# Kernel optimization log

Hardware: AMD Instinct MI355X
Metric: run time of the kernel (lower is better)

Reference implementation:

```python
import jax, jax.numpy as jnp
import numpy as np

B1, B2, D = 8192, 12288, 128


def setup_inputs() -> dict:
    key = jax.random.key(0)
    k1, k2 = jax.random.split(key)
    desc1 = jax.random.normal(k1, (B1, D), dtype=jnp.float32)
    desc2 = jax.random.normal(k2, (B2, D), dtype=jnp.float32)
    return {"desc1": desc1, "desc2": desc2}


def reference(desc1, desc2):
    # Pairwise L2 distance (torch.cdist, p=2) via the expanded form to avoid
    sq1 = jnp.sum(desc1 * desc1, axis=1, keepdims=True)          # (B1, 1)
    sq2 = jnp.sum(desc2 * desc2, axis=1)                          # (B2,)
    cost = jnp.sqrt(jnp.maximum(sq1 + sq2 - 2.0 * (desc1 @ desc2.T), 0.0))  # (B1, B2)

    b1, b2 = cost.shape
    ms = min(b1, b2)

    match_dists = jnp.min(cost, axis=1)    # (B1,) row minima
    idxs_in_2 = jnp.argmin(cost, axis=1)   # (B1,)
    match_dists2 = jnp.min(cost, axis=0)   # (B2,) col minima
    idxs_in_1 = jnp.argmin(cost, axis=0)   # (B2,)

    minsize_idxs = jnp.arange(ms)
    if b1 <= b2:  # static shape comparison -> Python if is fine
        mutual_nns = minsize_idxs == idxs_in_1[idxs_in_2][:ms]
        dists = match_dists[:ms]
        matches_idxs = jnp.stack([minsize_idxs, idxs_in_2[:ms]], axis=1)
    else:
        mutual_nns = minsize_idxs == idxs_in_2[idxs_in_1][:ms]
        dists = match_dists2[:ms]
        matches_idxs = jnp.stack([idxs_in_1[:ms], minsize_idxs], axis=1)

    # jit-compatible fixed-size output: non-mutual rows are masked with
    # dist=+inf and idx=-1 instead of boolean-compressed as in torch.
    match_dists_out = jnp.where(mutual_nns, dists, jnp.inf).reshape(-1, 1)  # (ms, 1)
    matches_idxs_out = jnp.where(mutual_nns[:, None], matches_idxs, -1)      # (ms, 2)
    return match_dists_out, matches_idxs_out, mutual_nns
```

## Files before the change

### kernel.cpp

```cpp
#include <hip/hip_runtime.h>
#include <math.h>

#define NB1 8192
#define NB2 12288
#define DD  128

typedef unsigned long long u64;
typedef unsigned short ushort_t;
typedef __attribute__((ext_vector_type(8))) short short8;
typedef __attribute__((ext_vector_type(8))) _Float16 half8;
typedef __attribute__((ext_vector_type(4))) float f32x4;

__device__ __forceinline__ float bigf() { return __uint_as_float(0x7F7F0000u); }
__device__ __forceinline__ u64 umin64(u64 a, u64 b) { return a < b ? a : b; }
__device__ __forceinline__ unsigned umin32(unsigned a, unsigned b) { return a < b ? a : b; }

__device__ __forceinline__ ushort_t bf_rn(float x) {
    unsigned u = __float_as_uint(x);
    return (ushort_t)((u + 0x7FFFu + ((u >> 16) & 1u)) >> 16);
}
__device__ __forceinline__ float bf_up(ushort_t h) {
    return __uint_as_float(((unsigned)h) << 16);
}
__device__ __forceinline__ int fswz(int r) { return (r + (r >> 2)) & 3; }
__device__ __forceinline__ half8 ld8h(const _Float16* p) { return *(const half8*)p; }

__global__ __launch_bounds__(256) void prep_kernel(
    const float* __restrict__ d1, const float* __restrict__ d2,
    float* __restrict__ sq1, float* __restrict__ sq2,
    u64* __restrict__ rowmin, u64* __restrict__ colmin) {
    int t = blockIdx.x * 256 + threadIdx.x;
    if (t < NB1) {
        rowmin[t] = ~0ull;
        const float4* p = (const float4*)(d1 + (size_t)t * DD);
        float s = 0.f;
        #pragma unroll
        for (int c = 0; c < DD / 4; ++c) {
            float4 v = p[c];
            s = fmaf(v.x, v.x, s); s = fmaf(v.y, v.y, s);
            s = fmaf(v.z, v.z, s); s = fmaf(v.w, v.w, s);
        }
        sq1[t] = s;
    }
    if (t < NB2) {
        colmin[t] = ~0ull;
        const float4* p = (const float4*)(d2 + (size_t)t * DD);
        float s = 0.f;
        #pragma unroll
        for (int c = 0; c < DD / 4; ++c) {
            float4 v = p[c];
            s = fmaf(v.x, v.x, s); s = fmaf(v.y, v.y, s);
            s = fmaf(v.z, v.z, s); s = fmaf(v.w, v.w, s);
        }
        sq2[t] = s;
    }
}

__global__ __launch_bounds__(256) void split_ext16_kernel(
    const float* __restrict__ d1, const float* __restrict__ d2,
    _Float16* __restrict__ Af, _Float16* __restrict__ Bf) {
    int t = blockIdx.x * 256 + threadIdx.x;
    int lane = t & 63;
    int task = t >> 6;
    bool isA = task < 6144;
    int lt = isA ? task : task - 6144;
    int rb = lt / 12;
    int kc = lt - rb * 12;
    int region = kc >> 2;
    int row = rb * 16 + (lane & 15);
    int kst = (kc & 3) * 32 + (lane >> 4) * 8;
    const float* src = (isA ? d1 : d2) + (size_t)row * DD + kst;
    _Float16* dst = (isA ? Af : Bf) + ((size_t)lt * 512 + lane * 8);

    bool wantM = isA ? (region == 1) : (region == 2);
    half8 V;
    #pragma unroll
    for (int e = 0; e < 8; ++e) {
        float x = src[e];
        _Float16 hf = (_Float16)x;
        float h = (float)hf;
        float v;
        if (region == 0)      v = x;
        else if (wantM)       v = (x - h) * 256.0f;
        else                  v = h * 0.00390625f;
        V[e] = (_Float16)v;
    }
    *(half8*)dst = V;
}

__global__ __launch_bounds__(256) void mfma_tile8_kernel(
    const _Float16* __restrict__ Af, const _Float16* __restrict__ Bf,
    const float* __restrict__ sq1, const float* __restrict__ sq2,
    u64* __restrict__ rowmin, u64* __restrict__ colmin)
{
    const int bid  = blockIdx.x;
    const int xcd  = bid & 7;
    const int t_   = bid >> 3;
    const int kch  = t_ >> 6;
    const int wdn  = t_ & 63;
    const int j0b  = (kch * 8 + (wdn & 7)) * 128;
    const int i0b  = (xcd * 8 + (wdn >> 3)) * 128;

    const int tid  = threadIdx.x;
    const int lane = tid & 63;
    const int wid  = tid >> 6;
    const int wr   = wid >> 1;
    const int wc   = wid & 1;
    const int lrow = lane & 15;
    const int lg   = lane >> 4;

    const _Float16* abase = Af + ((size_t)((i0b >> 4) + wr * 4) * 6144) + lane * 8;
    const _Float16* bbase = Bf + ((size_t)((j0b >> 4) + wc * 4) * 6144) + lane * 8;

    f32x4 acc[4][4];
    #pragma unroll
    for (int mi = 0; mi < 4; ++mi)
        #pragma unroll
        for (int ni = 0; ni < 4; ++ni)
            acc[mi][ni] = (f32x4){0.f, 0.f, 0.f, 0.f};

    #pragma unroll 1
    for (int kc = 0; kc < 12; ++kc) {
        const int ko = kc * 512;
        half8 bfr[4];
        #pragma unroll
        for (int ni = 0; ni < 4; ++ni)
            bfr[ni] = ld8h(bbase + ni * 6144 + ko);
        half8 a0, a1;
        a0 = ld8h(abase + ko);
        #pragma unroll
        for (int mi = 0; mi < 4; ++mi) {
            if (mi < 3)
                a1 = ld8h(abase + (mi + 1) * 6144 + ko);
            #pragma unroll
            for (int ni = 0; ni < 4; ++ni)
                acc[mi][ni] = __builtin_amdgcn_mfma_f32_16x16x32_f16(a0, bfr[ni], acc[mi][ni], 0, 0, 0);
            a0 = a1;
        }
    }

    float q2v[4];
    #pragma unroll
    for (int ni = 0; ni < 4; ++ni)
        q2v[ni] = sq2[j0b + wc * 64 + ni * 16 + lrow];
    float4 q1v[4];
    #pragma unroll
    for (int mi = 0; mi < 4; ++mi)
        q1v[mi] = *(const float4*)(sq1 + i0b + wr * 64 + mi * 16 + 4 * lg);

    float    cmin[4];
    unsigned cidx[4];
    #pragma unroll
    for (int ni = 0; ni < 4; ++ni) { cmin[ni] = __uint_as_float(0x7F800000u); cidx[ni] = 0xFFFFFFFFu; }

    #pragma unroll
    for (int mi = 0; mi < 4; ++mi) {
        const float* q1p = (const float*)&q1v[mi];
        #pragma unroll
        for (int r = 0; r < 4; ++r) {
            const float    q1 = q1p[r];
            const unsigned irow = (unsigned)(i0b + wr * 64 + mi * 16 + 4 * lg + r);
            float    rbest = 0.f;
            unsigned rbn = 0;
            #pragma unroll
            for (int ni = 0; ni < 4; ++ni) {
                float d = acc[mi][ni][r];
                float t = fmaf(-2.f, d, q2v[ni]);
                float c = fmaf(-2.f, d, q1);
                if (ni == 0) { rbest = t; }
                else if (t < rbest) { rbest = t; rbn = (unsigned)ni; }
                if (c < cmin[ni]) { cmin[ni] = c; cidx[ni] = irow; }
            }
            float g = rbest;
            #pragma unroll
            for (int mask = 8; mask; mask >>= 1)
                g = fminf(g, __shfl_xor(g, mask));
            unsigned jc = (rbest == g)
                ? (unsigned)(j0b + wc * 64 + rbn * 16 + lrow) : 0xFFFFFFFFu;
            #pragma unroll
            for (int mask = 8; mask; mask >>= 1)
                jc = umin32(jc, (unsigned)__shfl_xor((int)jc, mask));
            if (lrow == 0) {
                float d2 = g + q1;
                u64 pk = ((u64)__float_as_uint(d2) << 32) | jc;
                atomicMin(&rowmin[irow], pk);
            }
        }
    }

    #pragma unroll
    for (int ni = 0; ni < 4; ++ni) {
        float d2 = cmin[ni] + q2v[ni];
        u64 pk = ((u64)__float_as_uint(d2) << 32) | cidx[ni];
        pk = umin64(pk, __shfl_xor(pk, 16));
        pk = umin64(pk, __shfl_xor(pk, 32));
        if (lane < 16)
            atomicMin(&colmin[j0b + wc * 64 + ni * 16 + lrow], pk);
    }
}

__global__ __launch_bounds__(256) void mfma_tile_kernel(
    const float* __restrict__ d1, const float* __restrict__ d2,
    const float* __restrict__ sq1, const float* __restrict__ sq2,
    u64* __restrict__ rowmin, u64* __restrict__ colmin)
{
    __shared__ __align__(16) short lds[6 * 4096];
    const int tid = threadIdx.x;
    const int i0b = blockIdx.y * 128;
    const int j0b = blockIdx.x * 128;
    const int srow  = tid >> 1;
    const int shalf = tid & 1;
    const int sfr   = fswz(srow);
    const int sg0   = ((2 * shalf) ^ sfr) * 8;
    const int sg1   = ((2 * shalf + 1) ^ sfr) * 8;
    const float* gA = d1 + (size_t)(i0b + srow) * DD + shalf * 16;
    const float* gB = d2 + (size_t)(j0b + srow) * DD + shalf * 16;
    short* wA = lds + srow * 32;
    short* wB = lds + 3 * 4096 + srow * 32;
    const int lane = tid & 63;
    const int wid  = tid >> 6;
    const int wr   = wid >> 1;
    const int wc   = wid & 1;
    const int lrow = lane & 15;
    const int lg   = lane >> 4;
    const int gx   = (lg ^ fswz(lrow)) * 8;
    const int aoff = (wr * 64 + lrow) * 32 + gx;
    const int boff = 3 * 4096 + (wc * 64 + lrow) * 32 + gx;

    f32x4 acc[4][4];
    #pragma unroll
    for (int mi = 0; mi < 4; ++mi)
        #pragma unroll
        for (int ni = 0; ni < 4; ++ni)
            acc[mi][ni] = (f32x4){0.f, 0.f, 0.f, 0.f};

    for (int kc = 0; kc < 4; ++kc) {
        {
            const float* sp = gA + kc * 32;
            short8 H0, M0, L0, H1, M1, L1;
            #pragma unroll
            for (int e = 0; e < 8; ++e) {
                float x = sp[e];
                ushort_t h = bf_rn(x); float r1 = x - bf_up(h);
                ushort_t m = bf_rn(r1); float r2 = r1 - bf_up(m);
                H0[e] = (short)h; M0[e] = (short)m; L0[e] = (short)bf_rn(r2);
            }
            #pragma unroll
            for (int e = 0; e < 8; ++e) {
                float x = sp[8 + e];
                ushort_t h = bf_rn(x); float r1 = x - bf_up(h);
                ushort_t m = bf_rn(r1); float r2 = r1 - bf_up(m);
                H1[e] = (short)h; M1[e] = (short)m; L1[e] = (short)bf_rn(r2);
            }
            *(short8*)(wA + sg0)        = H0;
            *(short8*)(wA + sg1)        = H1;
            *(short8*)(wA + 4096 + sg0) = M0;
            *(short8*)(wA + 4096 + sg1) = M1;
            *(short8*)(wA + 8192 + sg0) = L0;
            *(short8*)(wA + 8192 + sg1) = L1;
        }
        {
            const float* sp = gB + kc * 32;
            short8 H0, M0, L0, H1, M1, L1;
            #pragma unroll
            for (int e = 0; e < 8; ++e) {
                float x = sp[e];
                ushort_t h = bf_rn(x); float r1 = x - bf_up(h);
                ushort_t m = bf_rn(r1); float r2 = r1 - bf_up(m);
                H0[e] = (short)h; M0[e] = (short)m; L0[e] = (short)bf_rn(r2);
            }
            #pragma unroll
            for (int e = 0; e < 8; ++e) {
                float x = sp[8 + e];
                ushort_t h = bf_rn(x); float r1 = x - bf_up(h);
                ushort_t m = bf_rn(r1); float r2 = r1 - bf_up(m);
                H1[e] = (short)h; M1[e] = (short)m; L1[e] = (short)bf_rn(r2);
            }
            *(short8*)(wB + sg0)        = H0;
            *(short8*)(wB + sg1)        = H1;
            *(short8*)(wB + 4096 + sg0) = M0;
            *(short8*)(wB + 4096 + sg1) = M1;
            *(short8*)(wB + 8192 + sg0) = L0;
            *(short8*)(wB + 8192 + sg1) = L1;
        }
        __syncthreads();
        short8 af[3][4], bfr[3][4];
        #pragma unroll
        for (int c = 0; c < 3; ++c)
            #pragma unroll
            for (int t = 0; t < 4; ++t) {
                af[c][t]  = *(const short8*)(lds + c * 4096 + aoff + t * 512);
                bfr[c][t] = *(const short8*)(lds + c * 4096 + boff + t * 512);
            }
        #pragma unroll
        for (int mi = 0; mi < 4; ++mi)
            #pragma unroll
            for (int ni = 0; ni < 4; ++ni) {
                f32x4 a = acc[mi][ni];
                a = __builtin_amdgcn_mfma_f32_16x16x32_bf16(af[0][mi], bfr[0][ni], a, 0, 0, 0);
                a = __builtin_amdgcn_mfma_f32_16x16x32_bf16(af[0][mi], bfr[1][ni], a, 0, 0, 0);
                a = __builtin_amdgcn_mfma_f32_16x16x32_bf16(af[1][mi], bfr[0][ni], a, 0, 0, 0);
                a = __builtin_amdgcn_mfma_f32_16x16x32_bf16(af[0][mi], bfr[2][ni], a, 0, 0, 0);
                a = __builtin_amdgcn_mfma_f32_16x16x32_bf16(af[1][mi], bfr[1][ni], a, 0, 0, 0);
                a = __builtin_amdgcn_mfma_f32_16x16x32_bf16(af[2][mi], bfr[0][ni], a, 0, 0, 0);
                acc[mi][ni] = a;
            }
        __syncthreads();
    }

    float q2v[4];
    #pragma unroll
    for (int ni = 0; ni < 4; ++ni)
        q2v[ni] = sq2[j0b + wc * 64 + ni * 16 + lrow];
    float4 q1v[4];
    #pragma unroll
    for (int mi = 0; mi < 4; ++mi)
        q1v[mi] = *(const float4*)(sq1 + i0b + wr * 64 + mi * 16 + 4 * lg);

    float    cmin[4];
    unsigned cidx[4];
    #pragma unroll
    for (int ni = 0; ni < 4; ++ni) { cmin[ni] = __uint_as_float(0x7F800000u); cidx[ni] = 0xFFFFFFFFu; }

    #pragma unroll
    for (int mi = 0; mi < 4; ++mi) {
        const float* q1p = (const float*)&q1v[mi];
        #pragma unroll
        for (int r = 0; r < 4; ++r) {
            const float    q1 = q1p[r];
            const unsigned irow = (unsigned)(i0b + wr * 64 + mi * 16 + 4 * lg + r);
            float    rbest = 0.f;
            unsigned rbn = 0;
            #pragma unroll
            for (int ni = 0; ni < 4; ++ni) {
                float d = acc[mi][ni][r];
                float t = fmaf(-2.f, d, q2v[ni]);
                float c = fmaf(-2.f, d, q1);
                if (ni == 0) { rbest = t; }
                else if (t < rbest) { rbest = t; rbn = (unsigned)ni; }
                if (c < cmin[ni]) { cmin[ni] = c; cidx[ni] = irow; }
            }
            float g = rbest;
            #pragma unroll
            for (int mask = 8; mask; mask >>= 1)
                g = fminf(g, __shfl_xor(g, mask));
            unsigned jc = (rbest == g)
                ? (unsigned)(j0b + wc * 64 + rbn * 16 + lrow) : 0xFFFFFFFFu;
            #pragma unroll
            for (int mask = 8; mask; mask >>= 1)
                jc = umin32(jc, (unsigned)__shfl_xor((int)jc, mask));
            if (lrow == 0) {
                float d2 = g + q1;
                u64 pk = ((u64)__float_as_uint(d2) << 32) | jc;
                atomicMin(&rowmin[irow], pk);
            }
        }
    }
    #pragma unroll
    for (int ni = 0; ni < 4; ++ni) {
        float d2 = cmin[ni] + q2v[ni];
        u64 pk = ((u64)__float_as_uint(d2) << 32) | cidx[ni];
        pk = umin64(pk, __shfl_xor(pk, 16));
        pk = umin64(pk, __shfl_xor(pk, 32));
        if (lane < 16)
            atomicMin(&colmin[j0b + wc * 64 + ni * 16 + lrow], pk);
    }
}

__global__ __launch_bounds__(256) void final_kernel(
    const u64* __restrict__ rowmin, const u64* __restrict__ colmin,
    float* __restrict__ out) {
    int i = blockIdx.x * 256 + threadIdx.x;
    if (i >= NB1) return;
    u64 rm = rowmin[i];
    unsigned ju = (unsigned)(rm & 0xFFFFFFFFu);
    float d2 = __uint_as_float((unsigned)(rm >> 32));
    float dist = sqrtf(fmaxf(d2, 0.f));
    dist = fminf(dist, bigf());
    bool valid = (ju < (unsigned)NB2);
    int j = valid ? (int)ju : 0;
    u64 cm = colmin[j];
    int i2 = (int)(cm & 0xFFFFFFFFu);
    bool mut = valid && (i2 == i);
    out[i] = mut ? dist : bigf();
    out[NB1 + 2 * i]     = mut ? (float)i : -1.f;
    out[NB1 + 2 * i + 1] = mut ? (float)j : -1.f;
    out[NB1 + 2 * NB1 + i] = mut ? 1.f : 0.f;
}

extern "C" void kernel_launch(void* const* d_in, const int* in_sizes, int n_in,
                              void* d_out, int out_size, void* d_ws, size_t ws_size,
                              hipStream_t stream) {
    const float* d1 = (const float*)d_in[0];
    const float* d2 = (const float*)d_in[1];
    float* out = (float*)d_out;

    char* ws = (char*)d_ws;
    float* sq1    = (float*)(ws);
    float* sq2    = (float*)(ws + 32768);
    u64*   rowmin = (u64*)(ws + 81920);
    u64*   colmin = (u64*)(ws + 147456);
    _Float16* Af = (_Float16*)(ws + 245760);
    _Float16* Bf = (_Float16*)(ws + 245760 + 6291456);
    const size_t need = 245760 + 6291456 + 9437184;

    hipLaunchKernelGGL(prep_kernel, dim3((NB2 + 255) / 256), dim3(256), 0, stream,
                       d1, d2, sq1, sq2, rowmin, colmin);
    if (ws_size >= need) {
        hipLaunchKernelGGL(split_ext16_kernel, dim3(3840), dim3(256), 0, stream,
                           d1, d2, Af, Bf);
        hipLaunchKernelGGL(mfma_tile8_kernel, dim3(6144), dim3(256), 0, stream,
                           Af, Bf, sq1, sq2, rowmin, colmin);
    } else {
        hipLaunchKernelGGL(mfma_tile_kernel, dim3(NB2 / 128, NB1 / 128), dim3(256), 0, stream,
                           d1, d2, sq1, sq2, rowmin, colmin);
    }
    hipLaunchKernelGGL(final_kernel, dim3((NB1 + 255) / 256), dim3(256), 0, stream,
                       rowmin, colmin, out);
}
```

Measured before the change: 230.2 us.

## Stage fp16 split operands through LDS via direct global-to-LDS loads

The split kernel now writes each descriptor as one row-major 384-wide fp16 row, with the high part and the two scaled residual parts laid side by side. Before, the data was pre-packed into MFMA-fragment blocks. The GEMM kernel now uses global_load_lds to stage a 128x32 A tile and a 128x32 B tile per K step into swizzled shared memory, and all four waves read their fragments from there. The goal is to cut redundant global/L2 fragment loads, since previously each fragment was fetched separately by two waves. The cost is two block barriers per K step with a single LDS buffer and no overlap of load and compute.

```diff
diff --git a/kernel.cpp b/kernel.cpp
--- a/kernel.cpp
+++ b/kernel.cpp
@@ -4,6 +4,7 @@
 #define NB1 8192
 #define NB2 12288
 #define DD  128
+#define KE  384
 
 typedef unsigned long long u64;
 typedef unsigned short ushort_t;
@@ -24,6 +25,12 @@
 }
 __device__ __forceinline__ int fswz(int r) { return (r + (r >> 2)) & 3; }
 __device__ __forceinline__ half8 ld8h(const _Float16* p) { return *(const half8*)p; }
+
+__device__ __forceinline__ void gload_lds16(const void* g, void* l) {
+    __builtin_amdgcn_global_load_lds(
+        (const __attribute__((address_space(1))) unsigned*)g,
+        (__attribute__((address_space(3))) unsigned*)l, 16, 0, 0);
+}
 
 __global__ __launch_bounds__(256) void prep_kernel(
     const float* __restrict__ d1, const float* __restrict__ d2,
@@ -56,43 +63,43 @@
     }
 }
 
-__global__ __launch_bounds__(256) void split_ext16_kernel(
+__global__ __launch_bounds__(256) void split_kcat16_kernel(
     const float* __restrict__ d1, const float* __restrict__ d2,
-    _Float16* __restrict__ Af, _Float16* __restrict__ Bf) {
+    _Float16* __restrict__ Ap, _Float16* __restrict__ Bp) {
     int t = blockIdx.x * 256 + threadIdx.x;
-    int lane = t & 63;
-    int task = t >> 6;
-    bool isA = task < 6144;
-    int lt = isA ? task : task - 6144;
-    int rb = lt / 12;
-    int kc = lt - rb * 12;
-    int region = kc >> 2;
-    int row = rb * 16 + (lane & 15);
-    int kst = (kc & 3) * 32 + (lane >> 4) * 8;
-    const float* src = (isA ? d1 : d2) + (size_t)row * DD + kst;
-    _Float16* dst = (isA ? Af : Bf) + ((size_t)lt * 512 + lane * 8);
-
-    bool wantM = isA ? (region == 1) : (region == 2);
-    half8 V;
-    #pragma unroll
-    for (int e = 0; e < 8; ++e) {
-        float x = src[e];
-        _Float16 hf = (_Float16)x;
-        float h = (float)hf;
-        float v;
-        if (region == 0)      v = x;
-        else if (wantM)       v = (x - h) * 256.0f;
-        else                  v = h * 0.00390625f;
-        V[e] = (_Float16)v;
-    }
-    *(half8*)dst = V;
-}
-
-__global__ __launch_bounds__(256) void mfma_tile8_kernel(
-    const _Float16* __restrict__ Af, const _Float16* __restrict__ Bf,
+    int row = t >> 2, q = t & 3;
+    bool isA = row < NB1;
+    int r = isA ? row : row - NB1;
+    const float* src = (isA ? d1 : d2) + (size_t)r * DD + q * 32;
+    _Float16* dst = (isA ? Ap : Bp) + (size_t)r * KE + q * 32;
+
+    #pragma unroll
+    for (int v = 0; v < 4; ++v) {
+        half8 H, S1, S2;
+        #pragma unroll
+        for (int e = 0; e < 8; ++e) {
+            float x = src[v * 8 + e];
+            _Float16 hf = (_Float16)x;
+            float h = (float)hf;
+            _Float16 Mt = (_Float16)((x - h) * 256.0f);
+            _Float16 Ht = (_Float16)(h * 0.00390625f);
+            H[e] = hf;
+            S1[e] = isA ? Mt : Ht;
+            S2[e] = isA ? Ht : Mt;
+        }
+        *(half8*)(dst + v * 8)       = H;
+        *(half8*)(dst + 128 + v * 8) = S1;
+        *(half8*)(dst + 256 + v * 8) = S2;
+    }
+}
+
+__global__ __launch_bounds__(256) void mfma_lds9_kernel(
+    const _Float16* __restrict__ Ap, const _Float16* __restrict__ Bp,
     const float* __restrict__ sq1, const float* __restrict__ sq2,
     u64* __restrict__ rowmin, u64* __restrict__ colmin)
 {
+    __shared__ __align__(16) _Float16 lds[8192];
+
     const int bid  = blockIdx.x;
     const int xcd  = bid & 7;
     const int t_   = bid >> 3;
@@ -109,8 +116,23 @@
     const int lrow = lane & 15;
     const int lg   = lane >> 4;
 
-    const _Float16* abase = Af + ((size_t)((i0b >> 4) + wr * 4) * 6144) + lane * 8;
-    const _Float16* bbase = Bf + ((size_t)((j0b >> 4) + wc * 4) * 6144) + lane * 8;
+    const int srow0 = wid * 16 + (lane >> 2);
+    const int srow1 = 64 + srow0;
+    const int g0 = (lane & 3) ^ ((srow0 >> 1) & 3);
+    const int g1 = (lane & 3) ^ ((srow1 >> 1) & 3);
+    const _Float16* a0src = Ap + (size_t)(i0b + srow0) * KE + g0 * 8;
+    const _Float16* a1src = Ap + (size_t)(i0b + srow1) * KE + g1 * 8;
+    const _Float16* b0src = Bp + (size_t)(j0b + srow0) * KE + g0 * 8;
+    const _Float16* b1src = Bp + (size_t)(j0b + srow1) * KE + g1 * 8;
+    char* ldsA0 = (char*)lds + wid * 1024;
+    char* ldsA1 = (char*)lds + 4096 + wid * 1024;
+    char* ldsB0 = (char*)lds + 8192 + wid * 1024;
+    char* ldsB1 = (char*)lds + 12288 + wid * 1024;
+
+    const int arow = wr * 64 + lrow;
+    const int brow = wc * 64 + lrow;
+    const int aoff = arow * 32 + ((lg ^ ((arow >> 1) & 3)) * 8);
+    const int boff = 4096 + brow * 32 + ((lg ^ ((brow >> 1) & 3)) * 8);
 
     f32x4 acc[4][4];
     #pragma unroll
@@ -120,23 +142,27 @@
             acc[mi][ni] = (f32x4){0.f, 0.f, 0.f, 0.f};
 
     #pragma unroll 1
-    for (int kc = 0; kc < 12; ++kc) {
-        const int ko = kc * 512;
-        half8 bfr[4];
+    for (int T = 0; T < 12; ++T) {
+        const int ko = T * 32;
+        gload_lds16(a0src + ko, ldsA0);
+        gload_lds16(a1src + ko, ldsA1);
+        gload_lds16(b0src + ko, ldsB0);
+        gload_lds16(b1src + ko, ldsB1);
+        __syncthreads();
+
+        half8 aF[4], bF[4];
+        #pragma unroll
+        for (int mi = 0; mi < 4; ++mi)
+            aF[mi] = ld8h(lds + aoff + mi * 512);
         #pragma unroll
         for (int ni = 0; ni < 4; ++ni)
-            bfr[ni] = ld8h(bbase + ni * 6144 + ko);
-        half8 a0, a1;
-        a0 = ld8h(abase + ko);
-        #pragma unroll
-        for (int mi = 0; mi < 4; ++mi) {
-            if (mi < 3)
-                a1 = ld8h(abase + (mi + 1) * 6144 + ko);
+            bF[ni] = ld8h(lds + boff + ni * 512);
+        #pragma unroll
+        for (int mi = 0; mi < 4; ++mi)
             #pragma unroll
             for (int ni = 0; ni < 4; ++ni)
-                acc[mi][ni] = __builtin_amdgcn_mfma_f32_16x16x32_f16(a0, bfr[ni], acc[mi][ni], 0, 0, 0);
-            a0 = a1;
-        }
+                acc[mi][ni] = __builtin_amdgcn_mfma_f32_16x16x32_f16(aF[mi], bF[ni], acc[mi][ni], 0, 0, 0);
+        __syncthreads();
     }
 
     float q2v[4];
@@ -187,7 +213,6 @@
             }
         }
     }
-
     #pragma unroll
     for (int ni = 0; ni < 4; ++ni) {
         float d2 = cmin[ni] + q2v[ni];
@@ -400,17 +425,17 @@
     float* sq2    = (float*)(ws + 32768);
     u64*   rowmin = (u64*)(ws + 81920);
     u64*   colmin = (u64*)(ws + 147456);
-    _Float16* Af = (_Float16*)(ws + 245760);
-    _Float16* Bf = (_Float16*)(ws + 245760 + 6291456);
+    _Float16* Ap = (_Float16*)(ws + 245760);
+    _Float16* Bp = (_Float16*)(ws + 245760 + 6291456);
     const size_t need = 245760 + 6291456 + 9437184;
 
     hipLaunchKernelGGL(prep_kernel, dim3((NB2 + 255) / 256), dim3(256), 0, stream,
                        d1, d2, sq1, sq2, rowmin, colmin);
     if (ws_size >= need) {
-        hipLaunchKernelGGL(split_ext16_kernel, dim3(3840), dim3(256), 0, stream,
-                           d1, d2, Af, Bf);
-        hipLaunchKernelGGL(mfma_tile8_kernel, dim3(6144), dim3(256), 0, stream,
-                           Af, Bf, sq1, sq2, rowmin, colmin);
+        hipLaunchKernelGGL(split_kcat16_kernel, dim3(320), dim3(256), 0, stream,
+                           d1, d2, Ap, Bp);
+        hipLaunchKernelGGL(mfma_lds9_kernel, dim3(6144), dim3(256), 0, stream,
+                           Ap, Bp, sq1, sq2, rowmin, colmin);
     } else {
         hipLaunchKernelGGL(mfma_tile_kernel, dim3(NB2 / 128, NB1 / 128), dim3(256), 0, stream,
                            d1, d2, sq1, sq2, rowmin, colmin);
```

Result: faster. 222.5 us (-3.3%).

## Replace global atomicMin with per-tile partial minima and a separate reduce pass

Applied to the files above, without the earlier changes.

The distance tile kernel no longer does 64-bit atomicMin on the global row and column minima. Each block now combines its two warp halves in shared memory and writes one partial minimum per row and per column into a partial buffer. A new reduce kernel then scans 96 partials per row and 64 partials per column. The aim is to remove atomic contention on the global minima, at the cost of about 12 MB of extra global traffic, one more kernel launch, and a larger workspace requirement; when the workspace is too small the launcher falls back to other paths.

```diff
diff --git a/kernel.cpp b/kernel.cpp
--- a/kernel.cpp
+++ b/kernel.cpp
@@ -4,6 +4,8 @@
 #define NB1 8192
 #define NB2 12288
 #define DD  128
+#define NJB 96
+#define NIB 64
 
 typedef unsigned long long u64;
 typedef unsigned short ushort_t;
@@ -88,11 +90,14 @@
     *(half8*)dst = V;
 }
 
-__global__ __launch_bounds__(256) void mfma_tile8_kernel(
+__global__ __launch_bounds__(256) void mfma_tile10_kernel(
     const _Float16* __restrict__ Af, const _Float16* __restrict__ Bf,
     const float* __restrict__ sq1, const float* __restrict__ sq2,
-    u64* __restrict__ rowmin, u64* __restrict__ colmin)
+    u64* __restrict__ rowpart, u64* __restrict__ colpart)
 {
+    __shared__ u64 rowbuf[2][128];
+    __shared__ u64 colbuf[2][128];
+
     const int bid  = blockIdx.x;
     const int xcd  = bid & 7;
     const int t_   = bid >> 3;
@@ -182,12 +187,11 @@
                 jc = umin32(jc, (unsigned)__shfl_xor((int)jc, mask));
             if (lrow == 0) {
                 float d2 = g + q1;
-                u64 pk = ((u64)__float_as_uint(d2) << 32) | jc;
-                atomicMin(&rowmin[irow], pk);
-            }
-        }
-    }
-
+                rowbuf[wc][wr * 64 + mi * 16 + 4 * lg + r] =
+                    ((u64)__float_as_uint(d2) << 32) | jc;
+            }
+        }
+    }
     #pragma unroll
     for (int ni = 0; ni < 4; ++ni) {
         float d2 = cmin[ni] + q2v[ni];
@@ -195,7 +199,39 @@
         pk = umin64(pk, __shfl_xor(pk, 16));
         pk = umin64(pk, __shfl_xor(pk, 32));
         if (lane < 16)
-            atomicMin(&colmin[j0b + wc * 64 + ni * 16 + lrow], pk);
+            colbuf[wr][wc * 64 + ni * 16 + lrow] = pk;
+    }
+    __syncthreads();
+
+    const int jb = j0b >> 7;
+    const int ib = i0b >> 7;
+    if (tid < 128) {
+        u64 pk = umin64(rowbuf[0][tid], rowbuf[1][tid]);
+        rowpart[(size_t)jb * NB1 + i0b + tid] = pk;
+    } else {
+        int c = tid - 128;
+        u64 pk = umin64(colbuf[0][c], colbuf[1][c]);
+        colpart[(size_t)ib * NB2 + j0b + c] = pk;
+    }
+}
+
+__global__ __launch_bounds__(256) void reduce_kernel(
+    const u64* __restrict__ rowpart, const u64* __restrict__ colpart,
+    u64* __restrict__ rowmin, u64* __restrict__ colmin) {
+    int t = blockIdx.x * 256 + threadIdx.x;
+    if (t < NB1) {
+        u64 m = ~0ull;
+        #pragma unroll 8
+        for (int jb = 0; jb < NJB; ++jb)
+            m = umin64(m, rowpart[(size_t)jb * NB1 + t]);
+        rowmin[t] = m;
+    } else if (t < NB1 + NB2) {
+        int j = t - NB1;
+        u64 m = ~0ull;
+        #pragma unroll 8
+        for (int ib = 0; ib < NIB; ++ib)
+            m = umin64(m, colpart[(size_t)ib * NB2 + j]);
+        colmin[j] = m;
     }
 }
 
@@ -402,15 +438,25 @@
     u64*   colmin = (u64*)(ws + 147456);
     _Float16* Af = (_Float16*)(ws + 245760);
     _Float16* Bf = (_Float16*)(ws + 245760 + 6291456);
-    const size_t need = 245760 + 6291456 + 9437184;
+    u64* rowpart = (u64*)(ws + 15974400);
+    u64* colpart = (u64*)(ws + 15974400 + 6291456);
+    const size_t need2 = 15974400 + 2 * 6291456;
+    const size_t need1 = 245760 + 6291456 + 9437184;
 
     hipLaunchKernelGGL(prep_kernel, dim3((NB2 + 255) / 256), dim3(256), 0, stream,
                        d1, d2, sq1, sq2, rowmin, colmin);
-    if (ws_size >= need) {
+    if (ws_size >= need2) {
         hipLaunchKernelGGL(split_ext16_kernel, dim3(3840), dim3(256), 0, stream,
                            d1, d2, Af, Bf);
-        hipLaunchKernelGGL(mfma_tile8_kernel, dim3(6144), dim3(256), 0, stream,
-                           Af, Bf, sq1, sq2, rowmin, colmin);
+        hipLaunchKernelGGL(mfma_tile10_kernel, dim3(6144), dim3(256), 0, stream,
+                           Af, Bf, sq1, sq2, rowpart, colpart);
+        hipLaunchKernelGGL(reduce_kernel, dim3((NB1 + NB2 + 255) / 256), dim3(256), 0, stream,
+                           rowpart, colpart, rowmin, colmin);
+    } else if (ws_size >= need1) {
+        hipLaunchKernelGGL(split_ext16_kernel, dim3(3840), dim3(256), 0, stream,
+                           d1, d2, Af, Bf);
+        hipLaunchKernelGGL(mfma_tile_kernel, dim3(NB2 / 128, NB1 / 128), dim3(256), 0, stream,
+                           d1, d2, sq1, sq2, rowmin, colmin);
     } else {
         hipLaunchKernelGGL(mfma_tile_kernel, dim3(NB2 / 128, NB1 / 128), dim3(256), 0, stream,
                            d1, d2, sq1, sq2, rowmin, colmin);
```

Measured after the change: 227.0 us. About the same (-1.4%).
